# Kernel optimization log

Hardware: AMD Instinct MI355X
Metric: run time of the kernel (lower is better)

## Reference

```python
import jax, jax.numpy as jnp
import numpy as np

NUM_CLASSES = 10
IGNORE_BACKGROUND = True
WEIGH_BY_CLASS_SIZE = True


def setup_inputs() -> dict:
    key = jax.random.key(0)
    k1, k2 = jax.random.split(key)
    shape = (4, 1, 160, 160, 160)
    y_pred = jax.random.randint(k1, shape, 0, NUM_CLASSES, dtype=jnp.int32)
    y_true = jax.random.randint(k2, shape, 0, NUM_CLASSES, dtype=jnp.int32)
    return {"y_pred": y_pred, "y_true": y_true}


def reference(y_pred, y_true):
    n = y_pred.shape[0]
    C = NUM_CLASSES
    yp = y_pred.reshape(n, -1)  # [n, V]
    yt = y_true.reshape(n, -1)  # [n, V]

    # One fused batched histogram: key = batch_index * C + label
    offs = (jnp.arange(n, dtype=jnp.int32) * C)[:, None]  # [n, 1]
    kp = (yp + offs).ravel()
    kt = (yt + offs).ravel()
    ones = jnp.ones(kp.shape, dtype=jnp.float32)

    c_pred = jax.ops.segment_sum(ones, kp, num_segments=n * C).reshape(n, C)
    c_true = jax.ops.segment_sum(ones, kt, num_segments=n * C).reshape(n, C)
    match = (yp == yt).ravel().astype(jnp.float32)
    intersection = jax.ops.segment_sum(match, kp, num_segments=n * C).reshape(n, C)

    denom = c_pred + c_true
    if IGNORE_BACKGROUND:
        intersection = intersection[:, 1:]
        denom = denom[:, 1:]
        c_pred = c_pred[:, 1:]
        c_true = c_true[:, 1:]

    nonzero = denom > 0
    denom_safe = jnp.where(nonzero, denom, 1.0)
    dice_terms = jnp.where(nonzero, 2.0 * intersection / denom_safe, 0.0)

    if WEIGH_BY_CLASS_SIZE:
        weight = c_true / c_true.sum(-1, keepdims=True) / n
        return (1.0 - jnp.sum(jnp.where(nonzero, weight, 0.0) * dice_terms)).astype(jnp.float32)
    else:
        cnt = jnp.sum(nonzero)
        return (1.0 - jnp.sum(dice_terms) / cnt).astype(jnp.float32)
```

## Files before the change

### kernel.cpp

```cpp
#include <hip/hip_runtime.h>

#define NB 4
#define NC 9
#define BATCH_ELEMS (160*160*160)
#define NVEC (BATCH_ELEMS/4)
#define BPB 500
#define THREADS 256
#define TPB_BATCH (BPB*THREADS)
#define VEC_PER_THREAD (NVEC/TPB_BATCH)
#define NBLK (NB*BPB)
#define NPACK 14


__device__ __forceinline__ void proc(int a, int b,
                                     unsigned long long& accP,
                                     unsigned long long& accT,
                                     unsigned long long& accI)
{
    unsigned long long sa = 1ull << (6 * a);
    unsigned long long sb = 1ull << (6 * b);
    accP += sa;
    accT += sb;
    accI += (a == b) ? sa : 0ull;
}

__global__ __launch_bounds__(THREADS, 8) void dice_hist_kernel(
    const int* __restrict__ y_pred,
    const int* __restrict__ y_true,
    unsigned int* __restrict__ cnt)
{
    const int batch = blockIdx.x / BPB;
    const int bIn   = blockIdx.x % BPB;
    const int4* __restrict__ p = (const int4*)(y_pred + (size_t)batch * BATCH_ELEMS);
    const int4* __restrict__ t = (const int4*)(y_true + (size_t)batch * BATCH_ELEMS);
    const int tid = bIn * THREADS + threadIdx.x;

    unsigned long long accP = 0ull, accT = 0ull, accI = 0ull;

    #pragma unroll
    for (int k = 0; k < VEC_PER_THREAD; k += 2) {
        int4 a0 = p[tid + k * TPB_BATCH];
        int4 b0 = t[tid + k * TPB_BATCH];
        int4 a1 = p[tid + (k + 1) * TPB_BATCH];
        int4 b1 = t[tid + (k + 1) * TPB_BATCH];
        proc(a0.x, b0.x, accP, accT, accI);
        proc(a0.y, b0.y, accP, accT, accI);
        proc(a0.z, b0.z, accP, accT, accI);
        proc(a0.w, b0.w, accP, accT, accI);
        proc(a1.x, b1.x, accP, accT, accI);
        proc(a1.y, b1.y, accP, accT, accI);
        proc(a1.z, b1.z, accP, accT, accI);
        proc(a1.w, b1.w, accP, accT, accI);
    }

    unsigned int packed[NPACK];
    #pragma unroll
    for (int j = 0; j < NPACK; ++j) {
        int k0 = 2 * j, k1 = 2 * j + 1;
        int c0 = (k0 % 9) + 1, t0 = k0 / 9;
        unsigned long long a0 = (t0 == 0) ? accP : (t0 == 1) ? accT : accI;
        unsigned int v0 = (unsigned int)((a0 >> (6 * c0)) & 63ull);
        unsigned int v1 = 0;
        if (k1 < 27) {
            int c1 = (k1 % 9) + 1, t1 = k1 / 9;
            unsigned long long a1 = (t1 == 0) ? accP : (t1 == 1) ? accT : accI;
            v1 = (unsigned int)((a1 >> (6 * c1)) & 63ull);
        }
        packed[j] = v0 | (v1 << 16);
    }

    #pragma unroll
    for (int off = 32; off > 0; off >>= 1) {
        #pragma unroll
        for (int j = 0; j < NPACK; ++j)
            packed[j] += __shfl_down(packed[j], off, 64);
    }

    __shared__ unsigned int swave[4][NPACK];
    const int wave = threadIdx.x >> 6;
    const int lane = threadIdx.x & 63;
    if (lane == 0) {
        #pragma unroll
        for (int j = 0; j < NPACK; ++j) swave[wave][j] = packed[j];
    }
    __syncthreads();
    if (threadIdx.x < NPACK) {
        unsigned int s = swave[0][threadIdx.x] + swave[1][threadIdx.x]
                       + swave[2][threadIdx.x] + swave[3][threadIdx.x];
        cnt[blockIdx.x * NPACK + threadIdx.x] = s;
    }
}

__global__ __launch_bounds__(256) void dice_finish_kernel(
    const unsigned int* __restrict__ cnt, float* __restrict__ out)
{
    __shared__ unsigned int tot[NB * 28];
    const int t = threadIdx.x;
    if (t < NB * 28) tot[t] = 0u;
    __syncthreads();

    if (t < 224) {
        const int g     = t >> 2;
        const int sub   = t & 3;
        const int batch = g / NPACK;
        const int j     = g % NPACK;
        unsigned int lo = 0, hi = 0;
        const int base = batch * BPB;
        const int b0 = sub * (BPB / 4), b1 = b0 + (BPB / 4);
        for (int b = b0; b < b1; ++b) {
            unsigned int v = cnt[(base + b) * NPACK + j];
            lo += v & 0xFFFFu;
            hi += v >> 16;
        }
        atomicAdd(&tot[batch * 28 + 2 * j], lo);
        atomicAdd(&tot[batch * 28 + 2 * j + 1], hi);
    }
    __syncthreads();

    if (t == 0) {
        float loss = 0.0f;
        for (int n = 0; n < NB; ++n) {
            const unsigned int* c = &tot[n * 28];
            float tsum = 0.0f;
            for (int i = 0; i < NC; ++i) tsum += (float)c[9 + i];
            for (int i = 0; i < NC; ++i) {
                float cp = (float)c[0 + i];
                float ct = (float)c[9 + i];
                float I  = (float)c[18 + i];
                float denom = cp + ct;
                if (denom > 0.0f)
                    loss += (ct / tsum / (float)NB) * (2.0f * I / denom);
            }
        }
        out[0] = 1.0f - loss;
    }
}

extern "C" void kernel_launch(void* const* d_in, const int* in_sizes, int n_in,
                              void* d_out, int out_size, void* d_ws, size_t ws_size,
                              hipStream_t stream) {
    const int* y_pred = (const int*)d_in[0];
    const int* y_true = (const int*)d_in[1];
    unsigned int* cnt = (unsigned int*)d_ws;

    dice_hist_kernel<<<NBLK, THREADS, 0, stream>>>(y_pred, y_true, cnt);
    dice_finish_kernel<<<1, 256, 0, stream>>>(cnt, (float*)d_out);
}
```

Measured before the change: 159.0 us.

## Double grid size, front-load loads, and reduce block partials with global atomics

Doubles the blocks per batch so each thread handles four int4 pairs, and issues all eight vector loads before any processing. Each block now unpacks its partial counts and atomically adds them into a small zeroed global total, replacing the per-block partial array and the serial reduction in the finish kernel. The intent is to raise memory-level parallelism and shorten the single-block tail. The cost is an extra memset launch and contention from thousands of atomics on 108 addresses.

```diff
diff --git a/kernel.cpp b/kernel.cpp
--- a/kernel.cpp
+++ b/kernel.cpp
@@ -4,10 +4,10 @@
 #define NC 9
 #define BATCH_ELEMS (160*160*160)
 #define NVEC (BATCH_ELEMS/4)
-#define BPB 500
+#define BPB 1000
 #define THREADS 256
 #define TPB_BATCH (BPB*THREADS)
-#define VEC_PER_THREAD (NVEC/TPB_BATCH)
+#define VPT 4
 #define NBLK (NB*BPB)
 #define NPACK 14
 
@@ -27,7 +27,7 @@
 __global__ __launch_bounds__(THREADS, 8) void dice_hist_kernel(
     const int* __restrict__ y_pred,
     const int* __restrict__ y_true,
-    unsigned int* __restrict__ cnt)
+    unsigned int* __restrict__ tot)
 {
     const int batch = blockIdx.x / BPB;
     const int bIn   = blockIdx.x % BPB;
@@ -35,36 +35,45 @@
     const int4* __restrict__ t = (const int4*)(y_true + (size_t)batch * BATCH_ELEMS);
     const int tid = bIn * THREADS + threadIdx.x;
 
+    int4 a0 = p[tid + 0 * TPB_BATCH];
+    int4 a1 = p[tid + 1 * TPB_BATCH];
+    int4 a2 = p[tid + 2 * TPB_BATCH];
+    int4 a3 = p[tid + 3 * TPB_BATCH];
+    int4 b0 = t[tid + 0 * TPB_BATCH];
+    int4 b1 = t[tid + 1 * TPB_BATCH];
+    int4 b2 = t[tid + 2 * TPB_BATCH];
+    int4 b3 = t[tid + 3 * TPB_BATCH];
+
     unsigned long long accP = 0ull, accT = 0ull, accI = 0ull;
-
-    #pragma unroll
-    for (int k = 0; k < VEC_PER_THREAD; k += 2) {
-        int4 a0 = p[tid + k * TPB_BATCH];
-        int4 b0 = t[tid + k * TPB_BATCH];
-        int4 a1 = p[tid + (k + 1) * TPB_BATCH];
-        int4 b1 = t[tid + (k + 1) * TPB_BATCH];
-        proc(a0.x, b0.x, accP, accT, accI);
-        proc(a0.y, b0.y, accP, accT, accI);
-        proc(a0.z, b0.z, accP, accT, accI);
-        proc(a0.w, b0.w, accP, accT, accI);
-        proc(a1.x, b1.x, accP, accT, accI);
-        proc(a1.y, b1.y, accP, accT, accI);
-        proc(a1.z, b1.z, accP, accT, accI);
-        proc(a1.w, b1.w, accP, accT, accI);
-    }
+    proc(a0.x, b0.x, accP, accT, accI);
+    proc(a0.y, b0.y, accP, accT, accI);
+    proc(a0.z, b0.z, accP, accT, accI);
+    proc(a0.w, b0.w, accP, accT, accI);
+    proc(a1.x, b1.x, accP, accT, accI);
+    proc(a1.y, b1.y, accP, accT, accI);
+    proc(a1.z, b1.z, accP, accT, accI);
+    proc(a1.w, b1.w, accP, accT, accI);
+    proc(a2.x, b2.x, accP, accT, accI);
+    proc(a2.y, b2.y, accP, accT, accI);
+    proc(a2.z, b2.z, accP, accT, accI);
+    proc(a2.w, b2.w, accP, accT, accI);
+    proc(a3.x, b3.x, accP, accT, accI);
+    proc(a3.y, b3.y, accP, accT, accI);
+    proc(a3.z, b3.z, accP, accT, accI);
+    proc(a3.w, b3.w, accP, accT, accI);
 
     unsigned int packed[NPACK];
     #pragma unroll
     for (int j = 0; j < NPACK; ++j) {
         int k0 = 2 * j, k1 = 2 * j + 1;
         int c0 = (k0 % 9) + 1, t0 = k0 / 9;
-        unsigned long long a0 = (t0 == 0) ? accP : (t0 == 1) ? accT : accI;
-        unsigned int v0 = (unsigned int)((a0 >> (6 * c0)) & 63ull);
+        unsigned long long x0 = (t0 == 0) ? accP : (t0 == 1) ? accT : accI;
+        unsigned int v0 = (unsigned int)((x0 >> (6 * c0)) & 63ull);
         unsigned int v1 = 0;
         if (k1 < 27) {
             int c1 = (k1 % 9) + 1, t1 = k1 / 9;
-            unsigned long long a1 = (t1 == 0) ? accP : (t1 == 1) ? accT : accI;
-            v1 = (unsigned int)((a1 >> (6 * c1)) & 63ull);
+            unsigned long long x1 = (t1 == 0) ? accP : (t1 == 1) ? accT : accI;
+            v1 = (unsigned int)((x1 >> (6 * c1)) & 63ull);
         }
         packed[j] = v0 | (v1 << 16);
     }
@@ -84,43 +93,29 @@
         for (int j = 0; j < NPACK; ++j) swave[wave][j] = packed[j];
     }
     __syncthreads();
-    if (threadIdx.x < NPACK) {
-        unsigned int s = swave[0][threadIdx.x] + swave[1][threadIdx.x]
-                       + swave[2][threadIdx.x] + swave[3][threadIdx.x];
-        cnt[blockIdx.x * NPACK + threadIdx.x] = s;
+
+    if (threadIdx.x < 27) {
+        const int j = threadIdx.x >> 1;
+        const int h = threadIdx.x & 1;
+        unsigned int v = ((swave[0][j] >> (16 * h)) & 0xFFFFu)
+                       + ((swave[1][j] >> (16 * h)) & 0xFFFFu)
+                       + ((swave[2][j] >> (16 * h)) & 0xFFFFu)
+                       + ((swave[3][j] >> (16 * h)) & 0xFFFFu);
+        atomicAdd(&tot[batch * 27 + threadIdx.x], v);
     }
 }
 
-__global__ __launch_bounds__(256) void dice_finish_kernel(
-    const unsigned int* __restrict__ cnt, float* __restrict__ out)
+__global__ __launch_bounds__(128) void dice_finish_kernel(
+    const unsigned int* __restrict__ tot, float* __restrict__ out)
 {
-    __shared__ unsigned int tot[NB * 28];
+    __shared__ unsigned int s[NB * 27];
     const int t = threadIdx.x;
-    if (t < NB * 28) tot[t] = 0u;
+    if (t < NB * 27) s[t] = tot[t];
     __syncthreads();
-
-    if (t < 224) {
-        const int g     = t >> 2;
-        const int sub   = t & 3;
-        const int batch = g / NPACK;
-        const int j     = g % NPACK;
-        unsigned int lo = 0, hi = 0;
-        const int base = batch * BPB;
-        const int b0 = sub * (BPB / 4), b1 = b0 + (BPB / 4);
-        for (int b = b0; b < b1; ++b) {
-            unsigned int v = cnt[(base + b) * NPACK + j];
-            lo += v & 0xFFFFu;
-            hi += v >> 16;
-        }
-        atomicAdd(&tot[batch * 28 + 2 * j], lo);
-        atomicAdd(&tot[batch * 28 + 2 * j + 1], hi);
-    }
-    __syncthreads();
-
     if (t == 0) {
         float loss = 0.0f;
         for (int n = 0; n < NB; ++n) {
-            const unsigned int* c = &tot[n * 28];
+            const unsigned int* c = &s[n * 27];
             float tsum = 0.0f;
             for (int i = 0; i < NC; ++i) tsum += (float)c[9 + i];
             for (int i = 0; i < NC; ++i) {
@@ -141,8 +136,9 @@
                               hipStream_t stream) {
     const int* y_pred = (const int*)d_in[0];
     const int* y_true = (const int*)d_in[1];
-    unsigned int* cnt = (unsigned int*)d_ws;
+    unsigned int* tot = (unsigned int*)d_ws;
 
-    dice_hist_kernel<<<NBLK, THREADS, 0, stream>>>(y_pred, y_true, cnt);
-    dice_finish_kernel<<<1, 256, 0, stream>>>(cnt, (float*)d_out);
+    hipMemsetAsync(d_ws, 0, NB * 27 * sizeof(unsigned int), stream);
+    dice_hist_kernel<<<NBLK, THREADS, 0, stream>>>(y_pred, y_true, tot);
+    dice_finish_kernel<<<1, 128, 0, stream>>>(tot, (float*)d_out);
 }
```

New measurement: 161.2 us. Within noise of the previous version (+1.4%).
